# Kernel optimization log

Measured on AMD Instinct MI355X. Metric: run time of the kernel, lower is better.

## Reference

```python
import jax, jax.numpy as jnp
import numpy as np


def setup_inputs() -> dict:
    key = jax.random.key(0)
    ks = jax.random.split(key, 5)
    B, T, C = 2, 2048, 1024
    x = jax.random.normal(ks[0], (B, T, C), dtype=jnp.float32)
    Wqkv = jax.random.normal(ks[1], (C, 3 * C), dtype=jnp.float32) * (C ** -0.5)
    bqkv = jax.random.normal(ks[2], (3 * C,), dtype=jnp.float32) * 0.02
    Wproj = jax.random.normal(ks[3], (C, C), dtype=jnp.float32) * (C ** -0.5)
    bproj = jax.random.normal(ks[4], (C,), dtype=jnp.float32) * 0.02
    return {"x": x, "Wqkv": Wqkv, "bqkv": bqkv, "Wproj": Wproj, "bproj": bproj}


def reference(x, Wqkv, bqkv, Wproj, bproj):
    B, T, C = x.shape
    n_head = 16
    hd = C // n_head
    x_proj = x @ Wqkv + bqkv  # [B, T, 3C]
    # NOTE: source reshapes (B, T, C) -> (B, n_head, T, hd) directly (no transpose);
    # we replicate that exactly for faithfulness.
    q = x_proj[:, :, :C].reshape(B, n_head, T, hd)
    k = x_proj[:, :, C:2 * C].reshape(B, n_head, T, hd)
    v = x_proj[:, :, 2 * C:].reshape(B, n_head, T, hd)
    att = jnp.einsum('bhtd,bhsd->bhts', q, k) * (1.0 / jnp.sqrt(jnp.float32(hd)))
    causal = jnp.tril(jnp.ones((T, T), dtype=bool))  # True where allowed
    att = jnp.where(causal, att, jnp.float32(-jnp.inf))
    att = jax.nn.softmax(att, axis=-1)
    y = att @ v  # [B, H, T, hd]
    y = jnp.transpose(y, (0, 2, 1, 3)).reshape(B, T, C)
    return y @ Wproj + bproj
```

## Files before the change

### kernel.cpp

```cpp
#include <hip/hip_runtime.h>
#include <hip/hip_bf16.h>
#include <stdint.h>

typedef __hip_bfloat16 bf16;
typedef __attribute__((ext_vector_type(8))) short bf16x8;
typedef __attribute__((ext_vector_type(4))) float f32x4;

__device__ __forceinline__ bf16x8 ldsv8(const bf16* p) { return *(const bf16x8*)p; }

__device__ __forceinline__ short bf_bits(float f) {
  union { bf16 h; short s; } u; u.h = __float2bfloat16(f); return u.s;
}

#define QSCALE 0.18033688011112042f

#define ASYNC16(ldsdst, gsrc)                                                  \
  __builtin_amdgcn_global_load_lds(                                            \
      (const __attribute__((address_space(1))) void*)(gsrc),                   \
      (__attribute__((address_space(3))) void*)(ldsdst), 16, 0, 0)

__device__ __forceinline__ bool is_bf16(const void* p) {
  const uint32_t* w = (const uint32_t*)p;
  int cnt = 0;
#pragma unroll 8
  for (int i = 0; i < 64; ++i) {
    uint32_t e = (w[i] >> 7) & 0xffu;
    cnt += (e >= 100u && e <= 150u) ? 1 : 0;
  }
  return cnt >= 40;
}

__device__ __forceinline__ float load_f32(const void* p, size_t idx, bool b16) {
  return b16 ? __bfloat162float(((const bf16*)p)[idx]) : ((const float*)p)[idx];
}

__device__ __forceinline__ void cvtT_body(const void* in, bf16* out, int R,
                                          int Ccols, int bx, int by,
                                          bf16 (*tile)[33]) {
  const bool b16 = is_bf16(in);
  int tx = threadIdx.x & 31, ty = threadIdx.x >> 5;
  int c0 = bx * 32, r0 = by * 32;
#pragma unroll
  for (int i = 0; i < 32; i += 8)
    tile[ty + i][tx] = __float2bfloat16(load_f32(in, (size_t)(r0 + ty + i) * Ccols + c0 + tx, b16));
  __syncthreads();
#pragma unroll
  for (int i = 0; i < 32; i += 8)
    out[(size_t)(c0 + ty + i) * R + r0 + tx] = tile[tx][ty + i];
}

__global__ __launch_bounds__(256) void prep_k(const float* __restrict__ x,
                                              bf16* __restrict__ xb,
                                              const void* __restrict__ Wqkv,
                                              bf16* __restrict__ WqkvT,
                                              const void* __restrict__ Wproj,
                                              bf16* __restrict__ WprojT) {
  __shared__ __align__(16) bf16 tile[32][33];
  const int id = blockIdx.x;
  if (id < 2048) {
    size_t i = (size_t)id * 256 + threadIdx.x;
    const float4 f0 = ((const float4*)x)[i * 2];
    const float4 f1 = ((const float4*)x)[i * 2 + 1];
    bf16x8 pk = {bf_bits(f0.x), bf_bits(f0.y), bf_bits(f0.z), bf_bits(f0.w),
                 bf_bits(f1.x), bf_bits(f1.y), bf_bits(f1.z), bf_bits(f1.w)};
    ((bf16x8*)xb)[i] = pk;
  } else if (id < 5120) {
    int id2 = id - 2048;
    cvtT_body(Wqkv, WqkvT, 1024, 3072, id2 % 96, id2 / 96, tile);
  } else {
    int id3 = id - 5120;
    cvtT_body(Wproj, WprojT, 1024, 1024, id3 % 32, id3 / 32, tile);
  }
}

__global__ __launch_bounds__(256) void cvtT_k(const void* __restrict__ in,
                                              bf16* __restrict__ out,
                                              int R, int Ccols) {
  __shared__ __align__(16) bf16 tile[32][33];
  cvtT_body(in, out, R, Ccols, blockIdx.x, blockIdx.y, tile);
}

__global__ __launch_bounds__(256) void cvt_k(const float* __restrict__ in,
                                             bf16* __restrict__ out) {
  size_t i = (size_t)blockIdx.x * 256 + threadIdx.x;
  const float4 f0 = ((const float4*)in)[i * 2];
  const float4 f1 = ((const float4*)in)[i * 2 + 1];
  bf16x8 pk = {bf_bits(f0.x), bf_bits(f0.y), bf_bits(f0.z), bf_bits(f0.w),
               bf_bits(f1.x), bf_bits(f1.y), bf_bits(f1.z), bf_bits(f1.w)};
  ((bf16x8*)out)[i] = pk;
}

template <int MODE, int BN>
__global__ __launch_bounds__(256) void gemm128(
    const void* __restrict__ Araw, const bf16* __restrict__ BT,
    const void* __restrict__ biasraw, void* __restrict__ outv) {
  constexpr int K = 1024;
  constexpr int NBF = BN / 32;
  __shared__ __align__(16) bf16 As[128 * 32];
  __shared__ __align__(16) bf16 Bs[BN * 32];
  const int tid = threadIdx.x;
  const int wave = tid >> 6, lane = tid & 63;
  const int quad = lane >> 4, l16 = lane & 15;
  const int nwg = gridDim.x * gridDim.y;
  const int lin = blockIdx.y * gridDim.x + blockIdx.x;
  const int swz = (lin & 7) * (nwg >> 3) + (lin >> 3);
  const int m0 = (swz % gridDim.x) * 128, n0 = (swz / gridDim.x) * BN;
  const int wm = (wave & 1) * 64, wn = (wave >> 1) * (BN / 2);
  const bool a16 = (MODE == 0) ? is_bf16(Araw) : true;
  const bool bias16 = is_bf16(biasraw);

  f32x4 acc[4][NBF] = {};

  for (int kt = 0; kt < K; kt += 32) {
    __syncthreads();
    if (MODE != 0 || a16) {
#pragma unroll
      for (int i = 0; i < 2; ++i) {
        int slot = i * 256 + tid;
        int row = slot >> 2, col = (slot & 3) << 3;
        ASYNC16(As + slot * 8, ((const bf16*)Araw) + (size_t)(m0 + row) * K + kt + col);
      }
#pragma unroll
      for (int i = 0; i < BN / 64; ++i) {
        int slot = i * 256 + tid;
        int row = slot >> 2, col = (slot & 3) << 3;
        ASYNC16(Bs + slot * 8, BT + (size_t)(n0 + row) * K + kt + col);
      }
    } else {
#pragma unroll
      for (int i = 0; i < 2; ++i) {
        int slot = i * 256 + tid;
        int row = slot >> 2, col = (slot & 3) << 3;
        const float* ap = ((const float*)Araw) + (size_t)(m0 + row) * K + kt + col;
        float4 f0 = *(const float4*)ap;
        float4 f1 = *(const float4*)(ap + 4);
        bf16x8 pk = {bf_bits(f0.x), bf_bits(f0.y), bf_bits(f0.z), bf_bits(f0.w),
                     bf_bits(f1.x), bf_bits(f1.y), bf_bits(f1.z), bf_bits(f1.w)};
        *(bf16x8*)(As + slot * 8) = pk;
        if (i * 256 < BN * 4)
          *(bf16x8*)(Bs + slot * 8) = *(const bf16x8*)(BT + (size_t)(n0 + row) * K + kt + col);
      }
    }
    __syncthreads();
    bf16x8 af[4], bfr[NBF];
#pragma unroll
    for (int i = 0; i < 4; ++i)
      af[i] = ldsv8(As + (wm + i * 16 + l16) * 32 + quad * 8);
#pragma unroll
    for (int j = 0; j < NBF; ++j)
      bfr[j] = ldsv8(Bs + (wn + j * 16 + l16) * 32 + quad * 8);
#pragma unroll
    for (int i = 0; i < 4; ++i)
#pragma unroll
      for (int j = 0; j < NBF; ++j)
        acc[i][j] = __builtin_amdgcn_mfma_f32_16x16x32_bf16(af[i], bfr[j], acc[i][j], 0, 0, 0);
  }

  float biasf[NBF];
#pragma unroll
  for (int j = 0; j < NBF; ++j)
    biasf[j] = load_f32(biasraw, n0 + wn + j * 16 + l16, bias16);

#pragma unroll
  for (int i = 0; i < 4; ++i)
#pragma unroll
    for (int j = 0; j < NBF; ++j) {
      int ng = n0 + wn + j * 16 + l16;
#pragma unroll
      for (int r = 0; r < 4; ++r) {
        int mg = m0 + wm + i * 16 + quad * 4 + r;
        float v = acc[i][j][r] + biasf[j];
        if (MODE == 1) {
          ((float*)outv)[(size_t)mg * 1024 + ng] = v;
        } else {
          ((bf16*)outv)[(size_t)mg * 3072 + ng] =
              __float2bfloat16(ng < 1024 ? v * QSCALE : v);
        }
      }
    }
}

__global__ __launch_bounds__(512) void attn_k(const bf16* __restrict__ xproj,
                                              bf16* __restrict__ Yb) {
  constexpr int KSZ = 128 * 72;
  constexpr int VSZ = 64 * 136;
  __shared__ __align__(16) bf16 Ks[2 * KSZ];
  __shared__ __align__(16) bf16 VTs[2 * VSZ];
  __shared__ __align__(16) bf16 Ps[8 * 16 * 136];

  const int tid = threadIdx.x;
  const int wave = tid >> 6, lane = tid & 63;
  const int quad = lane >> 4, l16 = lane & 15;
  const int pid = blockIdx.x;
  const int qtA = pid, qtB = 15 - pid;
  const int bh = blockIdx.y, b = bh >> 4, h = bh & 15;
  const size_t rowbase = (size_t)(b * 2048 + h * 128) * 3072;
  const int q0[2] = {qtA * 128, qtB * 128};

  const short onebits = (short)0x3F80;
  const bf16x8 vones = {onebits, onebits, onebits, onebits,
                        onebits, onebits, onebits, onebits};

  bf16x8 aq[2][2];
#pragma unroll
  for (int t = 0; t < 2; ++t) {
    int sg = q0[t] + wave * 16 + l16;
    const bf16* qp = xproj + rowbase + (size_t)(sg >> 4) * 3072 + ((sg & 15) << 6);
#pragma unroll
    for (int ks = 0; ks < 2; ++ks)
      aq[t][ks] = *(const bf16x8*)(qp + ks * 32 + quad * 8);
  }

  f32x4 o[2][4] = {};
  f32x4 lacc[2] = {};

  bf16* Pw = Ps + wave * (16 * 136);

  const int slot0 = tid, slot1 = 512 + tid;
  const int sA = slot0 >> 3, blkA = slot0 & 7;
  const int sB = slot1 >> 3, blkB = slot1 & 7;

  bf16x8 kreg[2], vreg[2];
#define ISSUE_LOADS(stv)                                                        \
  {                                                                             \
    int sg0 = (stv)*128 + sA, sg1 = (stv)*128 + sB;                             \
    const bf16* b0 = xproj + rowbase + (size_t)(sg0 >> 4) * 3072 + ((sg0 & 15) << 6); \
    const bf16* b1 = xproj + rowbase + (size_t)(sg1 >> 4) * 3072 + ((sg1 & 15) << 6); \
    kreg[0] = *(const bf16x8*)(b0 + 1024 + blkA * 8);                           \
    vreg[0] = *(const bf16x8*)(b0 + 2048 + blkA * 8);                           \
    kreg[1] = *(const bf16x8*)(b1 + 1024 + blkB * 8);                           \
    vreg[1] = *(const bf16x8*)(b1 + 2048 + blkB * 8);                           \
  }
#define WRITE_TILE(buf)                                                         \
  {                                                                             \
    bf16* Kd = Ks + (buf)*KSZ;                                                  \
    bf16* Vd = VTs + (buf)*VSZ;                                                 \
    *(bf16x8*)(Kd + sA * 72 + blkA * 8) = kreg[0];                              \
    const bf16* ve0 = (const bf16*)&vreg[0];                                    \
    const int ssw0 = sA ^ (blkA << 3);                                          \
    _Pragma("unroll")                                                           \
    for (int j = 0; j < 8; ++j) Vd[(blkA * 8 + j) * 136 + ssw0] = ve0[j];       \
    *(bf16x8*)(Kd + sB * 72 + blkB * 8) = kreg[1];                              \
    const bf16* ve1 = (const bf16*)&vreg[1];                                    \
    const int ssw1 = sB ^ (blkB << 3);                                          \
    _Pragma("unroll")                                                           \
    for (int j = 0; j < 8; ++j) Vd[(blkB * 8 + j) * 136 + ssw1] = ve1[j];       \
  }

  ISSUE_LOADS(0);
  WRITE_TILE(0);
  ISSUE_LOADS(1);
  __syncthreads();

  int cur = 0;
  for (int st = 0; st <= qtB; ++st) {
    const bf16* Kc = Ks + cur * KSZ;
    const bf16* Vc = VTs + cur * VSZ;

    const bool doA = (st <= qtA);

    f32x4 sc0[8] = {}, sc1[8] = {};
    __builtin_amdgcn_s_setprio(1);
#pragma unroll
    for (int ks = 0; ks < 2; ++ks)
#pragma unroll
      for (int j = 0; j < 8; ++j) {
        bf16x8 bk = ldsv8(Kc + (j * 16 + l16) * 72 + (ks * 4 + quad) * 8);
        if (doA) sc0[j] = __builtin_amdgcn_mfma_f32_16x16x32_bf16(aq[0][ks], bk, sc0[j], 0, 0, 0);
        sc1[j] = __builtin_amdgcn_mfma_f32_16x16x32_bf16(aq[1][ks], bk, sc1[j], 0, 0, 0);
      }
    __builtin_amdgcn_s_setprio(0);

#pragma unroll
    for (int t = 0; t < 2; ++t) {
      if (t == 0 && !doA) continue;
      const f32x4* sc = (t == 0) ? sc0 : sc1;
      const bool diag = (st == (t == 0 ? qtA : qtB));

#pragma unroll
      for (int r = 0; r < 4; ++r) {
        const int rloc = wave * 16 + quad * 4 + r;
        bf16* prow = Pw + (quad * 4 + r) * 136;
        const int psw = quad << 3;
#pragma unroll
        for (int j = 0; j < 8; ++j) {
          float v = sc[j][r];
          if (diag && (j * 16 + l16) > rloc) v = -1e30f;
          prow[(j * 16 + l16) ^ psw] = __float2bfloat16(__builtin_amdgcn_exp2f(v));
        }
      }

      __builtin_amdgcn_s_setprio(1);
#pragma unroll
      for (int ks = 0; ks < 4; ++ks) {
        bf16x8 ap = ldsv8(Pw + l16 * 136 + (((ks * 4 + quad) ^ (l16 >> 2)) << 3));
        lacc[t] = __builtin_amdgcn_mfma_f32_16x16x32_bf16(ap, vones, lacc[t], 0, 0, 0);
#pragma unroll
        for (int j = 0; j < 4; ++j) {
          int d = j * 16 + l16;
          bf16x8 bv = ldsv8(Vc + d * 136 + (((ks * 4 + quad) ^ (2 * j + (l16 >> 3))) << 3));
          o[t][j] = __builtin_amdgcn_mfma_f32_16x16x32_bf16(ap, bv, o[t][j], 0, 0, 0);
        }
      }
      __builtin_amdgcn_s_setprio(0);
    }

    if (st < qtB) {
      WRITE_TILE(cur ^ 1);
      if (st + 2 <= qtB) ISSUE_LOADS(st + 2);
      __syncthreads();
      cur ^= 1;
    }
  }
#undef ISSUE_LOADS
#undef WRITE_TILE

  bf16* Yh = Yb + (size_t)b * 2097152 + h * 64;
#pragma unroll
  for (int t = 0; t < 2; ++t)
#pragma unroll
    for (int r = 0; r < 4; ++r) {
      int tt = q0[t] + wave * 16 + quad * 4 + r;
      float inv = 1.f / lacc[t][r];
#pragma unroll
      for (int j = 0; j < 4; ++j)
        Yh[(size_t)tt * 1024 + j * 16 + l16] = __float2bfloat16(o[t][j][r] * inv);
    }
}

extern "C" void kernel_launch(void* const* d_in, const int* in_sizes, int n_in,
                              void* d_out, int out_size, void* d_ws, size_t ws_size,
                              hipStream_t stream) {
  (void)out_size;
  const void* px     = d_in[0];
  const void* pWqkv  = (n_in > 1) ? d_in[1] : d_in[0];
  const void* pbqkv  = (n_in > 2) ? d_in[2] : d_in[0];
  const void* pWproj = (n_in > 3) ? d_in[3] : d_in[0];
  const void* pbproj = (n_in > 4) ? d_in[4] : d_in[0];
  for (int i = 0; i < n_in; ++i) {
    switch (in_sizes[i]) {
      case 4194304: px     = d_in[i]; break;
      case 3145728: pWqkv  = d_in[i]; break;
      case 3072:    pbqkv  = d_in[i]; break;
      case 1048576: pWproj = d_in[i]; break;
      case 1024:    pbproj = d_in[i]; break;
      default: break;
    }
  }

  char* ws = (char*)d_ws;
  bf16* xproj = (bf16*)(ws + 0);

  if (ws_size >= 41943040) {
    bf16* xb     = (bf16*)(ws + 25165824);
    bf16* WqkvT  = (bf16*)(ws + 33554432);
    bf16* WprojT = (bf16*)(ws + 39845888);
    bf16* Yb     = (bf16*)(ws + 27262976);

    prep_k<<<dim3(6144), 256, 0, stream>>>((const float*)px, xb, pWqkv, WqkvT,
                                           pWproj, WprojT);
    gemm128<0, 128><<<dim3(32, 24), 256, 0, stream>>>(xb, WqkvT, pbqkv, xproj);
    attn_k<<<dim3(8, 32), 512, 0, stream>>>(xproj, Yb);
    gemm128<1, 64><<<dim3(32, 16), 256, 0, stream>>>(Yb, WprojT, pbproj, d_out);
  } else if (ws_size >= 39845888) {
    bf16* xb     = (bf16*)(ws + 25165824);
    bf16* WqkvT  = (bf16*)(ws + 33554432);
    bf16* WprojT = (bf16*)(ws + 25165824);
    bf16* Yb     = (bf16*)(ws + 27262976);

    cvt_k<<<dim3(2048), 256, 0, stream>>>((const float*)px, xb);
    cvtT_k<<<dim3(96, 32), 256, 0, stream>>>(pWqkv, WqkvT, 1024, 3072);
    gemm128<0, 128><<<dim3(32, 24), 256, 0, stream>>>(xb, WqkvT, pbqkv, xproj);
    cvtT_k<<<dim3(32, 32), 256, 0, stream>>>(pWproj, WprojT, 1024, 1024);
    attn_k<<<dim3(8, 32), 512, 0, stream>>>(xproj, Yb);
    gemm128<1, 64><<<dim3(32, 16), 256, 0, stream>>>(Yb, WprojT, pbproj, d_out);
  } else {
    bf16* WqkvT  = (bf16*)(ws + 25165824);
    bf16* WprojT = (bf16*)(ws + 25165824);
    bf16* Yb     = (bf16*)(ws + 27262976);

    cvtT_k<<<dim3(96, 32), 256, 0, stream>>>(pWqkv, WqkvT, 1024, 3072);
    gemm128<0, 128><<<dim3(32, 24), 256, 0, stream>>>(px, WqkvT, pbqkv, xproj);
    cvtT_k<<<dim3(32, 32), 256, 0, stream>>>(pWproj, WprojT, 1024, 1024);
    attn_k<<<dim3(8, 32), 512, 0, stream>>>(xproj, Yb);
    gemm128<1, 64><<<dim3(32, 16), 256, 0, stream>>>(Yb, WprojT, pbproj, d_out);
  }
}
```

Measured before the change: 191.3 us.

## Split paired query tiles across two wave groups in 1024-thread attention blocks

```diff
diff --git a/kernel.cpp b/kernel.cpp
--- a/kernel.cpp
+++ b/kernel.cpp
@@ -180,71 +180,64 @@
     }
 }
 
-__global__ __launch_bounds__(512) void attn_k(const bf16* __restrict__ xproj,
-                                              bf16* __restrict__ Yb) {
+__global__ __launch_bounds__(1024, 4) void attn_k(const bf16* __restrict__ xproj,
+                                                  bf16* __restrict__ Yb) {
   constexpr int KSZ = 128 * 72;
   constexpr int VSZ = 64 * 136;
   __shared__ __align__(16) bf16 Ks[2 * KSZ];
   __shared__ __align__(16) bf16 VTs[2 * VSZ];
-  __shared__ __align__(16) bf16 Ps[8 * 16 * 136];
+  __shared__ __align__(16) bf16 Ps[16 * 16 * 136];
 
   const int tid = threadIdx.x;
   const int wave = tid >> 6, lane = tid & 63;
   const int quad = lane >> 4, l16 = lane & 15;
+  const int tl = wave >> 3;
+  const int wrow = (wave & 7) * 16;
   const int pid = blockIdx.x;
   const int qtA = pid, qtB = 15 - pid;
+  const int qt = tl ? qtB : qtA;
   const int bh = blockIdx.y, b = bh >> 4, h = bh & 15;
   const size_t rowbase = (size_t)(b * 2048 + h * 128) * 3072;
-  const int q0[2] = {qtA * 128, qtB * 128};
+  const int q0 = qt * 128;
 
   const short onebits = (short)0x3F80;
   const bf16x8 vones = {onebits, onebits, onebits, onebits,
                         onebits, onebits, onebits, onebits};
 
-  bf16x8 aq[2][2];
-#pragma unroll
-  for (int t = 0; t < 2; ++t) {
-    int sg = q0[t] + wave * 16 + l16;
+  bf16x8 aq[2];
+  {
+    int sg = q0 + wrow + l16;
     const bf16* qp = xproj + rowbase + (size_t)(sg >> 4) * 3072 + ((sg & 15) << 6);
 #pragma unroll
     for (int ks = 0; ks < 2; ++ks)
-      aq[t][ks] = *(const bf16x8*)(qp + ks * 32 + quad * 8);
-  }
-
-  f32x4 o[2][4] = {};
-  f32x4 lacc[2] = {};
+      aq[ks] = *(const bf16x8*)(qp + ks * 32 + quad * 8);
+  }
+
+  f32x4 o[4] = {};
+  f32x4 lacc = {};
 
   bf16* Pw = Ps + wave * (16 * 136);
 
-  const int slot0 = tid, slot1 = 512 + tid;
-  const int sA = slot0 >> 3, blkA = slot0 & 7;
-  const int sB = slot1 >> 3, blkB = slot1 & 7;
-
-  bf16x8 kreg[2], vreg[2];
+  const int sA = tid >> 3, blkA = tid & 7;
+
+  bf16x8 kreg, vreg;
 #define ISSUE_LOADS(stv)                                                        \
   {                                                                             \
-    int sg0 = (stv)*128 + sA, sg1 = (stv)*128 + sB;                             \
+    int sg0 = (stv)*128 + sA;                                                   \
     const bf16* b0 = xproj + rowbase + (size_t)(sg0 >> 4) * 3072 + ((sg0 & 15) << 6); \
-    const bf16* b1 = xproj + rowbase + (size_t)(sg1 >> 4) * 3072 + ((sg1 & 15) << 6); \
-    kreg[0] = *(const bf16x8*)(b0 + 1024 + blkA * 8);                           \
-    vreg[0] = *(const bf16x8*)(b0 + 2048 + blkA * 8);                           \
-    kreg[1] = *(const bf16x8*)(b1 + 1024 + blkB * 8);                           \
-    vreg[1] = *(const bf16x8*)(b1 + 2048 + blkB * 8);                           \
+    kreg = *(const bf16x8*)(b0 + 1024 + blkA * 8);                              \
+    vreg = *(const bf16x8*)(b0 + 2048 + blkA * 8);                              \
   }
 #define WRITE_TILE(buf)                                                         \
   {                                                                             \
     bf16* Kd = Ks + (buf)*KSZ;                                                  \
     bf16* Vd = VTs + (buf)*VSZ;                                                 \
-    *(bf16x8*)(Kd + sA * 72 + blkA * 8) = kreg[0];                              \
-    const bf16* ve0 = (const bf16*)&vreg[0];                                    \
-    const int ssw0 = sA ^ (blkA << 3);                                          \
+    *(bf16x8*)(Kd + sA * 72 + blkA * 8) = kreg;                                 \
+    const bf16* ve0 = (const bf16*)&kreg;  (void)ve0;                           \
+    const bf16* vv = (const bf16*)&vreg;                                        \
+    const int ssw = sA ^ (blkA << 3);                                           \
     _Pragma("unroll")                                                           \
-    for (int j = 0; j < 8; ++j) Vd[(blkA * 8 + j) * 136 + ssw0] = ve0[j];       \
-    *(bf16x8*)(Kd + sB * 72 + blkB * 8) = kreg[1];                              \
-    const bf16* ve1 = (const bf16*)&vreg[1];                                    \
-    const int ssw1 = sB ^ (blkB << 3);                                          \
-    _Pragma("unroll")                                                           \
-    for (int j = 0; j < 8; ++j) Vd[(blkB * 8 + j) * 136 + ssw1] = ve1[j];       \
+    for (int j = 0; j < 8; ++j) Vd[(blkA * 8 + j) * 136 + ssw] = vv[j];         \
   }
 
   ISSUE_LOADS(0);
@@ -257,29 +250,23 @@
     const bf16* Kc = Ks + cur * KSZ;
     const bf16* Vc = VTs + cur * VSZ;
 
-    const bool doA = (st <= qtA);
-
-    f32x4 sc0[8] = {}, sc1[8] = {};
-    __builtin_amdgcn_s_setprio(1);
-#pragma unroll
-    for (int ks = 0; ks < 2; ++ks)
-#pragma unroll
-      for (int j = 0; j < 8; ++j) {
-        bf16x8 bk = ldsv8(Kc + (j * 16 + l16) * 72 + (ks * 4 + quad) * 8);
-        if (doA) sc0[j] = __builtin_amdgcn_mfma_f32_16x16x32_bf16(aq[0][ks], bk, sc0[j], 0, 0, 0);
-        sc1[j] = __builtin_amdgcn_mfma_f32_16x16x32_bf16(aq[1][ks], bk, sc1[j], 0, 0, 0);
-      }
-    __builtin_amdgcn_s_setprio(0);
-
-#pragma unroll
-    for (int t = 0; t < 2; ++t) {
-      if (t == 0 && !doA) continue;
-      const f32x4* sc = (t == 0) ? sc0 : sc1;
-      const bool diag = (st == (t == 0 ? qtA : qtB));
+    if (st <= qt) {
+      const bool diag = (st == qt);
+
+      f32x4 sc[8] = {};
+      __builtin_amdgcn_s_setprio(1);
+#pragma unroll
+      for (int ks = 0; ks < 2; ++ks)
+#pragma unroll
+        for (int j = 0; j < 8; ++j) {
+          bf16x8 bk = ldsv8(Kc + (j * 16 + l16) * 72 + (ks * 4 + quad) * 8);
+          sc[j] = __builtin_amdgcn_mfma_f32_16x16x32_bf16(aq[ks], bk, sc[j], 0, 0, 0);
+        }
+      __builtin_amdgcn_s_setprio(0);
 
 #pragma unroll
       for (int r = 0; r < 4; ++r) {
-        const int rloc = wave * 16 + quad * 4 + r;
+        const int rloc = wrow + quad * 4 + r;
         bf16* prow = Pw + (quad * 4 + r) * 136;
         const int psw = quad << 3;
 #pragma unroll
@@ -294,12 +281,12 @@
 #pragma unroll
       for (int ks = 0; ks < 4; ++ks) {
         bf16x8 ap = ldsv8(Pw + l16 * 136 + (((ks * 4 + quad) ^ (l16 >> 2)) << 3));
-        lacc[t] = __builtin_amdgcn_mfma_f32_16x16x32_bf16(ap, vones, lacc[t], 0, 0, 0);
+        lacc = __builtin_amdgcn_mfma_f32_16x16x32_bf16(ap, vones, lacc, 0, 0, 0);
 #pragma unroll
         for (int j = 0; j < 4; ++j) {
           int d = j * 16 + l16;
           bf16x8 bv = ldsv8(Vc + d * 136 + (((ks * 4 + quad) ^ (2 * j + (l16 >> 3))) << 3));
-          o[t][j] = __builtin_amdgcn_mfma_f32_16x16x32_bf16(ap, bv, o[t][j], 0, 0, 0);
+          o[j] = __builtin_amdgcn_mfma_f32_16x16x32_bf16(ap, bv, o[j], 0, 0, 0);
         }
       }
       __builtin_amdgcn_s_setprio(0);
@@ -317,15 +304,13 @@
 
   bf16* Yh = Yb + (size_t)b * 2097152 + h * 64;
 #pragma unroll
-  for (int t = 0; t < 2; ++t)
-#pragma unroll
-    for (int r = 0; r < 4; ++r) {
-      int tt = q0[t] + wave * 16 + quad * 4 + r;
-      float inv = 1.f / lacc[t][r];
-#pragma unroll
-      for (int j = 0; j < 4; ++j)
-        Yh[(size_t)tt * 1024 + j * 16 + l16] = __float2bfloat16(o[t][j][r] * inv);
-    }
+  for (int r = 0; r < 4; ++r) {
+    int tt = q0 + wrow + quad * 4 + r;
+    float inv = 1.f / lacc[r];
+#pragma unroll
+    for (int j = 0; j < 4; ++j)
+      Yh[(size_t)tt * 1024 + j * 16 + l16] = __float2bfloat16(o[j][r] * inv);
+  }
 }
 
 extern "C" void kernel_launch(void* const* d_in, const int* in_sizes, int n_in,
@@ -360,7 +345,7 @@
     prep_k<<<dim3(6144), 256, 0, stream>>>((const float*)px, xb, pWqkv, WqkvT,
                                            pWproj, WprojT);
     gemm128<0, 128><<<dim3(32, 24), 256, 0, stream>>>(xb, WqkvT, pbqkv, xproj);
-    attn_k<<<dim3(8, 32), 512, 0, stream>>>(xproj, Yb);
+    attn_k<<<dim3(8, 32), 1024, 0, stream>>>(xproj, Yb);
     gemm128<1, 64><<<dim3(32, 16), 256, 0, stream>>>(Yb, WprojT, pbproj, d_out);
   } else if (ws_size >= 39845888) {
     bf16* xb     = (bf16*)(ws + 25165824);
@@ -372,7 +357,7 @@
     cvtT_k<<<dim3(96, 32), 256, 0, stream>>>(pWqkv, WqkvT, 1024, 3072);
     gemm128<0, 128><<<dim3(32, 24), 256, 0, stream>>>(xb, WqkvT, pbqkv, xproj);
     cvtT_k<<<dim3(32, 32), 256, 0, stream>>>(pWproj, WprojT, 1024, 1024);
-    attn_k<<<dim3(8, 32), 512, 0, stream>>>(xproj, Yb);
+    attn_k<<<dim3(8, 32), 1024, 0, stream>>>(xproj, Yb);
     gemm128<1, 64><<<dim3(32, 16), 256, 0, stream>>>(Yb, WprojT, pbproj, d_out);
   } else {
     bf16* WqkvT  = (bf16*)(ws + 25165824);
@@ -382,7 +367,7 @@
     cvtT_k<<<dim3(96, 32), 256, 0, stream>>>(pWqkv, WqkvT, 1024, 3072);
     gemm128<0, 128><<<dim3(32, 24), 256, 0, stream>>>(px, WqkvT, pbqkv, xproj);
     cvtT_k<<<dim3(32, 32), 256, 0, stream>>>(pWproj, WprojT, 1024, 1024);
-    attn_k<<<dim3(8, 32), 512, 0, stream>>>(xproj, Yb);
+    attn_k<<<dim3(8, 32), 1024, 0, stream>>>(xproj, Yb);
     gemm128<1, 64><<<dim3(32, 16), 256, 0, stream>>>(Yb, WprojT, pbproj, d_out);
   }
 }
```

After: 196.9 us. 1.03x slower.
